# Kernel optimization log

Hardware: AMD Instinct MI355X
Metric: run time of the kernel (lower is better)

## Reference

```python
import jax, jax.numpy as jnp
import numpy as np

B, IN, OUT, E, H, K = 8192, 1024, 256, 16, 512, 3
EPS = 1e-10


def setup_inputs() -> dict:
    key = jax.random.key(0)
    ks = jax.random.split(key, 5)
    scaled = lambda k, shape, fan: jax.random.normal(k, shape, jnp.float32) / np.sqrt(fan)
    return {
        "x": jax.random.normal(ks[0], (B, IN), jnp.float32),
        # torch init is zeros for w_gate (degenerate ties); use small random for a meaningful reference
        "w_gate": jax.random.normal(ks[1], (IN, E), jnp.float32) * 0.02,
        "W1": scaled(ks[2], (E, IN, H), IN),
        "b1": jnp.zeros((E, H), jnp.float32),
        "W2": scaled(ks[3], (E, H, OUT), H),
        "b2": jnp.zeros((E, OUT), jnp.float32),
    }


def _cv_squared(v):
    # torch .var() is unbiased (ddof=1)
    return jnp.var(v, ddof=1) / (jnp.mean(v) ** 2 + EPS)


def reference(x, w_gate, W1, b1, W2, b2):
    # --- top-k gating (eval mode: clean logits, no noise) ---
    logits = x @ w_gate                                   # [B, E]
    top_vals, top_idx = jax.lax.top_k(logits, K)          # [B, K]
    top_gates = jax.nn.softmax(top_vals, axis=-1)         # softmax over selected k
    rows = jnp.arange(logits.shape[0])[:, None]
    gates = jnp.zeros_like(logits).at[rows, top_idx].set(top_gates)  # sparse gates [B, E]

    # --- load-balancing loss ---
    importance = gates.sum(0)
    load = (gates > 0).sum(0).astype(jnp.float32)         # _gates_to_load (eval path)
    loss = _cv_squared(importance) + _cv_squared(load)

    # --- experts (MLP stand-in; dense compute, sparse combine via zero gates) ---
    h = jax.nn.relu(jnp.einsum('bi,eih->beh', x, W1) + b1)  # [B, E, H]
    expert_out = jnp.einsum('beh,eho->beo', h, W2) + b2     # [B, E, OUT]

    # combine: equivalent to SparseDispatcher gather/split/scatter-add with gate weighting
    y = jnp.einsum('be,beo->bo', gates, expert_out)         # [B, OUT]
    return y, loss
```

## Files before the change

### kernel.cpp

```cpp
#include <hip/hip_runtime.h>

#define B_ 8192
#define IN_ 1024
#define OUT_ 256
#define E_ 16
#define KTOP 3
#define H_ 512
#define MAXSLOTS 26624
#define NTILES 208
#define HBLK 16

typedef __bf16 bf16;
typedef __bf16 bf16x4 __attribute__((ext_vector_type(4)));
typedef __bf16 bf16x8 __attribute__((ext_vector_type(8)));
typedef float f32x4 __attribute__((ext_vector_type(4)));

__device__ __forceinline__ void async16(const bf16* g, bf16* l) {
    __builtin_amdgcn_global_load_lds(
        (const __attribute__((address_space(1))) void*)g,
        (__attribute__((address_space(3))) void*)l,
        16, 0, 0);
}

__global__ __launch_bounds__(256) void k_init(
    int* __restrict__ row_ids, int* __restrict__ tile_expert,
    bf16* __restrict__ zero_row,
    const float* __restrict__ wg, float* __restrict__ wgT) {
    int id = blockIdx.x * 256 + threadIdx.x;
    if (id < MAXSLOTS) row_ids[id] = -1;
    if (id < NTILES) tile_expert[id] = -1;
    if (id < IN_) zero_row[id] = (bf16)0.f;
    if (id < E_ * IN_) {
        int e = id >> 10, j = id & 1023;
        wgT[id] = wg[j * E_ + e];
    }
}

__global__ __launch_bounds__(256) void k_transpose(
    const float* __restrict__ W1, bf16* __restrict__ w1t,
    const float* __restrict__ W2, bf16* __restrict__ w2t) {
    __shared__ float tile[64][65];
    int bx = blockIdx.x;
    const float* in; bf16* out; int Kd, Nd, e, tk, tn;
    if (bx < 2048) {
        in = W1; out = w1t; Kd = IN_; Nd = H_;
        e = bx >> 7; int tt = bx & 127; tk = tt >> 3; tn = tt & 7;
    } else {
        bx -= 2048;
        in = W2; out = w2t; Kd = H_; Nd = OUT_;
        e = bx >> 5; int tt = bx & 31; tk = tt >> 2; tn = tt & 3;
    }
    int t = threadIdx.x;
    int r = t >> 6, c = t & 63;
    const float* src = in + ((size_t)e * Kd + tk * 64) * Nd + (size_t)tn * 64;
#pragma unroll
    for (int i = 0; i < 16; i++) {
        int rr = r + i * 4;
        tile[rr][c] = src[(size_t)rr * Nd + c];
    }
    __syncthreads();
    bf16* dst = out + ((size_t)e * Nd + tn * 64) * Kd + (size_t)tk * 64;
#pragma unroll
    for (int i = 0; i < 16; i++) {
        int rr = r + i * 4;
        dst[(size_t)rr * Kd + c] = (bf16)tile[c][rr];
    }
}

__global__ __launch_bounds__(256) void k_gating(
    const float* __restrict__ x, const float* __restrict__ wgT,
    bf16* __restrict__ xbf, int* __restrict__ top_idx, float* __restrict__ top_gate) {
    int t = threadIdx.x;
    int row = blockIdx.x * 4 + (t >> 6);
    int lane = t & 63;
    float acc[16];
#pragma unroll
    for (int e = 0; e < 16; e++) acc[e] = 0.f;
    const float4* x4p = (const float4*)(x + (size_t)row * IN_);
    const float4* w4 = (const float4*)wgT;
#pragma unroll
    for (int it = 0; it < 4; it++) {
        int j0 = it * 64 + lane;
        float4 xv = x4p[j0];
        bf16x4 xb;
        xb[0] = (bf16)xv.x; xb[1] = (bf16)xv.y; xb[2] = (bf16)xv.z; xb[3] = (bf16)xv.w;
        *(bf16x4*)(xbf + (size_t)row * IN_ + j0 * 4) = xb;
#pragma unroll
        for (int e = 0; e < 16; e++) {
            float4 wv = w4[e * 256 + j0];
            acc[e] += xv.x * wv.x + xv.y * wv.y + xv.z * wv.z + xv.w * wv.w;
        }
    }
#pragma unroll
    for (int e = 0; e < 16; e++) {
#pragma unroll
        for (int s = 32; s > 0; s >>= 1) acc[e] += __shfl_xor(acc[e], s, 64);
    }
    if (lane == 0) {
        float v[16];
#pragma unroll
        for (int e = 0; e < 16; e++) v[e] = acc[e];
        int idx[KTOP];
        float val[KTOP];
#pragma unroll
        for (int k = 0; k < KTOP; k++) {
            int best = 0;
            float bv = v[0];
            for (int e = 1; e < 16; e++) {
                if (v[e] > bv) { bv = v[e]; best = e; }
            }
            idx[k] = best; val[k] = bv; v[best] = -1e30f;
        }
        float e1 = __expf(val[1] - val[0]);
        float e2 = __expf(val[2] - val[0]);
        float inv = 1.f / (1.f + e1 + e2);
        float g[KTOP] = {inv, e1 * inv, e2 * inv};
#pragma unroll
        for (int k = 0; k < KTOP; k++) {
            top_idx[row * KTOP + k] = idx[k];
            top_gate[row * KTOP + k] = g[k];
        }
    }
}

__global__ __launch_bounds__(256) void k_hist(
    const int* __restrict__ top_idx, int* __restrict__ partial) {
    __shared__ int wcnt[4][16];
    int t = threadIdx.x;
    int w = t >> 6, lane = t & 63;
    int blk = blockIdx.x;
    int cnt[16];
#pragma unroll
    for (int k = 0; k < 16; k++) cnt[k] = 0;
#pragma unroll
    for (int j = 0; j < 6; j++) {
        int e = top_idx[blk * 1536 + j * 256 + t];
#pragma unroll
        for (int k = 0; k < 16; k++)
            cnt[k] += (int)__popcll(__ballot(e == k));
    }
    if (lane == 0) {
#pragma unroll
        for (int k = 0; k < 16; k++) wcnt[w][k] = cnt[k];
    }
    __syncthreads();
    if (t < 16) partial[blk * 16 + t] = wcnt[0][t] + wcnt[1][t] + wcnt[2][t] + wcnt[3][t];
}

__global__ __launch_bounds__(256) void k_scan(
    const int* __restrict__ partial, int* __restrict__ counts,
    int* __restrict__ tile_expert, int* __restrict__ gbase) {
    __shared__ int sp[HBLK * 16];
    __shared__ int soff[16];
    int t = threadIdx.x;
    sp[t] = partial[t];
    __syncthreads();
    if (t < 16) {
        int s = 0;
#pragma unroll
        for (int b = 0; b < HBLK; b++) s += sp[b * 16 + t];
        counts[t] = s;
    }
    __syncthreads();
    if (t == 0) {
        int off = 0;
        for (int e = 0; e < E_; e++) {
            int c = 0;
#pragma unroll
            for (int b = 0; b < HBLK; b++) c += sp[b * 16 + e];
            soff[e] = off;
            int pd = (c + 127) & ~127;
            int t0 = off >> 7, t1 = (off + pd) >> 7;
            for (int tt = t0; tt < t1; ++tt) tile_expert[tt] = e;
            off += pd;
        }
    }
    __syncthreads();
    {
        int b = t >> 4, e = t & 15;
        int s = soff[e];
        for (int bp = 0; bp < b; bp++) s += sp[bp * 16 + e];
        gbase[t] = s;
    }
}

__global__ __launch_bounds__(256) void k_scatter(
    const int* __restrict__ top_idx, const float* __restrict__ top_gate,
    const int* __restrict__ gbase,
    int* __restrict__ row_ids, int* __restrict__ rowslot,
    float* __restrict__ partial_imp) {
    __shared__ int lcnt[16];
    __shared__ float limp[16];
    int t = threadIdx.x;
    int blk = blockIdx.x;
    if (t < 16) { lcnt[t] = 0; limp[t] = 0.f; }
    __syncthreads();
#pragma unroll
    for (int j = 0; j < 6; j++) {
        int gid = blk * 1536 + j * 256 + t;
        int e = top_idx[gid];
        float g = top_gate[gid];
        int rank = atomicAdd(&lcnt[e], 1);
        atomicAdd(&limp[e], g);
        int slot = gbase[blk * 16 + e] + rank;
        row_ids[slot] = gid / KTOP;
        rowslot[gid] = slot;
    }
    __syncthreads();
    if (t < 16) partial_imp[blk * 16 + t] = limp[t];
}


__global__ __launch_bounds__(256) void k_gemm1(
    const bf16* __restrict__ xbf, const bf16* __restrict__ w1t,
    const float* __restrict__ b1, const int* __restrict__ row_ids,
    const int* __restrict__ tile_expert, const bf16* __restrict__ zero_row,
    bf16* __restrict__ h) {
    int e = tile_expert[blockIdx.y];
    if (e < 0) return;
    int slot_base = blockIdx.y * 128;
    int nbase = blockIdx.x * 128;
    __shared__ __align__(16) bf16 As[128 * 64];
    __shared__ __align__(16) bf16 Bs[128 * 64];
    int t = threadIdx.x;
    int rmod = (t >> 3) & 7;
    int cglob = (t & 7) ^ rmod;
    const bf16* gA[4];
    const bf16* gB[4];
#pragma unroll
    for (int j = 0; j < 4; j++) {
        int m = j * 32 + (t >> 3);
        int rid = row_ids[slot_base + m];
        gA[j] = ((rid >= 0) ? xbf + (size_t)rid * IN_ : zero_row) + cglob * 8;
        gB[j] = w1t + ((size_t)e * H_ + nbase + m) * IN_ + cglob * 8;
    }
    int w = t >> 6, lane = t & 63;
    int wm = (w >> 1) * 64, wn = (w & 1) * 64;
    int lm = lane & 15, lq = lane >> 4;
    f32x4 acc[4][4] = {};
    for (int k0 = 0; k0 < IN_; k0 += 64) {
#pragma unroll
        for (int j = 0; j < 4; j++) {
            async16(gA[j] + k0, As + (j * 256 + t) * 8);
            async16(gB[j] + k0, Bs + (j * 256 + t) * 8);
        }
        __syncthreads();
        const bf16x8* Av = (const bf16x8*)As;
        const bf16x8* Bv = (const bf16x8*)Bs;
#pragma unroll
        for (int ks = 0; ks < 2; ks++) {
            int kc = ks * 4 + lq;
            bf16x8 af[4], bfv[4];
#pragma unroll
            for (int i = 0; i < 4; i++) {
                int row = wm + i * 16 + lm;
                af[i] = Av[row * 8 + (kc ^ (row & 7))];
            }
#pragma unroll
            for (int i = 0; i < 4; i++) {
                int row = wn + i * 16 + lm;
                bfv[i] = Bv[row * 8 + (kc ^ (row & 7))];
            }
#pragma unroll
            for (int mi = 0; mi < 4; mi++)
#pragma unroll
                for (int ni = 0; ni < 4; ni++)
                    acc[mi][ni] = __builtin_amdgcn_mfma_f32_16x16x32_bf16(af[mi], bfv[ni], acc[mi][ni], 0, 0, 0);
        }
        __syncthreads();
    }
#pragma unroll
    for (int mi = 0; mi < 4; mi++) {
#pragma unroll
        for (int ni = 0; ni < 4; ni++) {
            int colg = nbase + wn + ni * 16 + lm;
            float bias = b1[e * H_ + colg];
#pragma unroll
            for (int r = 0; r < 4; r++) {
                int rowl = wm + mi * 16 + lq * 4 + r;
                float v = acc[mi][ni][r] + bias;
                v = v > 0.f ? v : 0.f;
                h[(size_t)(slot_base + rowl) * H_ + colg] = (bf16)v;
            }
        }
    }
}

__global__ __launch_bounds__(256) void k_gemm2(
    const bf16* __restrict__ h, const bf16* __restrict__ w2t,
    const float* __restrict__ b2, const int* __restrict__ tile_expert,
    float* __restrict__ eout) {
    int e = tile_expert[blockIdx.y];
    if (e < 0) return;
    int slot_base = blockIdx.y * 128;
    int nbase = blockIdx.x * 128;
    __shared__ __align__(16) bf16 As[128 * 64];
    __shared__ __align__(16) bf16 Bs[128 * 64];
    int t = threadIdx.x;
    int rmod = (t >> 3) & 7;
    int cglob = (t & 7) ^ rmod;
    const bf16* gA[4];
    const bf16* gB[4];
#pragma unroll
    for (int j = 0; j < 4; j++) {
        int m = j * 32 + (t >> 3);
        gA[j] = h + (size_t)(slot_base + m) * H_ + cglob * 8;
        gB[j] = w2t + ((size_t)e * OUT_ + nbase + m) * H_ + cglob * 8;
    }
    int w = t >> 6, lane = t & 63;
    int wm = (w >> 1) * 64, wn = (w & 1) * 64;
    int lm = lane & 15, lq = lane >> 4;
    f32x4 acc[4][4] = {};
    for (int k0 = 0; k0 < H_; k0 += 64) {
#pragma unroll
        for (int j = 0; j < 4; j++) {
            async16(gA[j] + k0, As + (j * 256 + t) * 8);
            async16(gB[j] + k0, Bs + (j * 256 + t) * 8);
        }
        __syncthreads();
        const bf16x8* Av = (const bf16x8*)As;
        const bf16x8* Bv = (const bf16x8*)Bs;
#pragma unroll
        for (int ks = 0; ks < 2; ks++) {
            int kc = ks * 4 + lq;
            bf16x8 af[4], bfv[4];
#pragma unroll
            for (int i = 0; i < 4; i++) {
                int row = wm + i * 16 + lm;
                af[i] = Av[row * 8 + (kc ^ (row & 7))];
            }
#pragma unroll
            for (int i = 0; i < 4; i++) {
                int row = wn + i * 16 + lm;
                bfv[i] = Bv[row * 8 + (kc ^ (row & 7))];
            }
#pragma unroll
            for (int mi = 0; mi < 4; mi++)
#pragma unroll
                for (int ni = 0; ni < 4; ni++)
                    acc[mi][ni] = __builtin_amdgcn_mfma_f32_16x16x32_bf16(af[mi], bfv[ni], acc[mi][ni], 0, 0, 0);
        }
        __syncthreads();
    }
#pragma unroll
    for (int mi = 0; mi < 4; mi++) {
#pragma unroll
        for (int ni = 0; ni < 4; ni++) {
            int colg = nbase + wn + ni * 16 + lm;
            float bias = b2[e * OUT_ + colg];
#pragma unroll
            for (int r = 0; r < 4; r++) {
                int rowl = wm + mi * 16 + lq * 4 + r;
                eout[(size_t)(slot_base + rowl) * OUT_ + colg] = acc[mi][ni][r] + bias;
            }
        }
    }
}

__global__ __launch_bounds__(256) void k_combine(
    const float* __restrict__ eout, const int* __restrict__ rowslot,
    const float* __restrict__ top_gate, float* __restrict__ y) {
    int t = threadIdx.x;
    int b = blockIdx.x * 4 + (t >> 6);
    int lane = t & 63;
    int s0 = rowslot[b * 3], s1 = rowslot[b * 3 + 1], s2 = rowslot[b * 3 + 2];
    float g0 = top_gate[b * 3], g1 = top_gate[b * 3 + 1], g2 = top_gate[b * 3 + 2];
    const float4* e4 = (const float4*)eout;
    float4 v0 = e4[(size_t)s0 * 64 + lane];
    float4 v1 = e4[(size_t)s1 * 64 + lane];
    float4 v2 = e4[(size_t)s2 * 64 + lane];
    float4 r;
    r.x = g0 * v0.x + g1 * v1.x + g2 * v2.x;
    r.y = g0 * v0.y + g1 * v1.y + g2 * v2.y;
    r.z = g0 * v0.z + g1 * v1.z + g2 * v2.z;
    r.w = g0 * v0.w + g1 * v1.w + g2 * v2.w;
    ((float4*)y)[(size_t)b * 64 + lane] = r;
}

__global__ void k_loss(const float* __restrict__ partial_imp, const int* __restrict__ counts,
                       float* __restrict__ loss_out) {
    __shared__ float imp[16];
    int t = threadIdx.x;
    if (t < 16) {
        float s = 0.f;
#pragma unroll
        for (int b = 0; b < HBLK; b++) s += partial_imp[b * 16 + t];
        imp[t] = s;
    }
    __syncthreads();
    if (t == 0) {
        float si = 0.f, sl = 0.f;
        for (int e = 0; e < E_; e++) { si += imp[e]; sl += (float)counts[e]; }
        float mi_ = si / (float)E_, ml_ = sl / (float)E_;
        float vi = 0.f, vl = 0.f;
        for (int e = 0; e < E_; e++) {
            float d = imp[e] - mi_; vi += d * d;
            float d2 = (float)counts[e] - ml_; vl += d2 * d2;
        }
        vi /= (float)(E_ - 1); vl /= (float)(E_ - 1);
        *loss_out = vi / (mi_ * mi_ + 1e-10f) + vl / (ml_ * ml_ + 1e-10f);
    }
}

extern "C" void kernel_launch(void* const* d_in, const int* in_sizes, int n_in,
                              void* d_out, int out_size, void* d_ws, size_t ws_size,
                              hipStream_t stream) {
    (void)in_sizes; (void)n_in; (void)out_size; (void)ws_size;
    const float* x = (const float*)d_in[0];
    const float* wgate = (const float*)d_in[1];
    const float* W1 = (const float*)d_in[2];
    const float* b1 = (const float*)d_in[3];
    const float* W2 = (const float*)d_in[4];
    const float* b2 = (const float*)d_in[5];
    float* y = (float*)d_out;

    char* p = (char*)d_ws;
    auto alloc = [&](size_t bytes) {
        char* q = p;
        p += (bytes + 255) & ~(size_t)255;
        return q;
    };
    bf16* xbf = (bf16*)alloc((size_t)B_ * IN_ * 2);
    bf16* w1t = (bf16*)alloc((size_t)E_ * H_ * IN_ * 2);
    bf16* w2t = (bf16*)alloc((size_t)E_ * OUT_ * H_ * 2);
    bf16* h = (bf16*)alloc((size_t)MAXSLOTS * H_ * 2);
    int* row_ids = (int*)alloc((size_t)MAXSLOTS * 4);
    int* rowslot = (int*)alloc((size_t)B_ * KTOP * 4);
    int* top_idx = (int*)alloc((size_t)B_ * KTOP * 4);
    float* top_gate = (float*)alloc((size_t)B_ * KTOP * 4);
    int* counts = (int*)alloc(E_ * 4);
    int* partial = (int*)alloc(HBLK * E_ * 4);
    int* gbase = (int*)alloc(HBLK * E_ * 4);
    float* partial_imp = (float*)alloc(HBLK * E_ * 4);
    int* tile_expert = (int*)alloc(NTILES * 4);
    bf16* zero_row = (bf16*)alloc(IN_ * 2);
    float* wgT = (float*)alloc((size_t)E_ * IN_ * 4);
    float* eout = (float*)xbf;

    k_init<<<dim3((MAXSLOTS + 255) / 256), dim3(256), 0, stream>>>(
        row_ids, tile_expert, zero_row, wgate, wgT);
    k_transpose<<<dim3(2048 + 512), dim3(256), 0, stream>>>(W1, w1t, W2, w2t);
    k_gating<<<dim3(B_ / 4), dim3(256), 0, stream>>>(x, wgT, xbf, top_idx, top_gate);
    k_hist<<<dim3(HBLK), dim3(256), 0, stream>>>(top_idx, partial);
    k_scan<<<dim3(1), dim3(256), 0, stream>>>(partial, counts, tile_expert, gbase);
    k_scatter<<<dim3(HBLK), dim3(256), 0, stream>>>(
        top_idx, top_gate, gbase, row_ids, rowslot, partial_imp);
    k_gemm1<<<dim3(H_ / 128, NTILES), dim3(256), 0, stream>>>(
        xbf, w1t, b1, row_ids, tile_expert, zero_row, h);
    k_gemm2<<<dim3(OUT_ / 128, NTILES), dim3(256), 0, stream>>>(
        h, w2t, b2, tile_expert, eout);
    k_combine<<<dim3(B_ / 4), dim3(256), 0, stream>>>(eout, rowslot, top_gate, y);
    k_loss<<<dim3(1), dim3(64), 0, stream>>>(partial_imp, counts, y + (size_t)B_ * OUT_);
}
```

Baseline: 221.3 us.

## Merge setup kernels, widen gemm2 tile, store expert outputs as bf16, fold loss

```diff
diff --git a/kernel.cpp b/kernel.cpp
--- a/kernel.cpp
+++ b/kernel.cpp
@@ -22,35 +22,37 @@
         16, 0, 0);
 }
 
-__global__ __launch_bounds__(256) void k_init(
-    int* __restrict__ row_ids, int* __restrict__ tile_expert,
-    bf16* __restrict__ zero_row,
-    const float* __restrict__ wg, float* __restrict__ wgT) {
-    int id = blockIdx.x * 256 + threadIdx.x;
-    if (id < MAXSLOTS) row_ids[id] = -1;
-    if (id < NTILES) tile_expert[id] = -1;
-    if (id < IN_) zero_row[id] = (bf16)0.f;
-    if (id < E_ * IN_) {
-        int e = id >> 10, j = id & 1023;
-        wgT[id] = wg[j * E_ + e];
-    }
-}
-
-__global__ __launch_bounds__(256) void k_transpose(
+__global__ __launch_bounds__(256) void k_setup(
     const float* __restrict__ W1, bf16* __restrict__ w1t,
-    const float* __restrict__ W2, bf16* __restrict__ w2t) {
+    const float* __restrict__ W2, bf16* __restrict__ w2t,
+    int* __restrict__ row_ids, const float* __restrict__ wg, float* __restrict__ wgT,
+    bf16* __restrict__ zero_row, int* __restrict__ tile_expert) {
+    int bx = blockIdx.x;
+    int t = threadIdx.x;
+    if (bx >= 2560) {
+        if (bx < 2664) {
+            row_ids[(bx - 2560) * 256 + t] = -1;
+        } else if (bx < 2728) {
+            int id = (bx - 2664) * 256 + t;
+            int e = id >> 10, j = id & 1023;
+            wgT[id] = wg[j * E_ + e];
+        } else {
+#pragma unroll
+            for (int i = 0; i < 4; i++) zero_row[t * 4 + i] = (bf16)0.f;
+            if (t < NTILES) tile_expert[t] = -1;
+        }
+        return;
+    }
     __shared__ float tile[64][65];
-    int bx = blockIdx.x;
     const float* in; bf16* out; int Kd, Nd, e, tk, tn;
     if (bx < 2048) {
         in = W1; out = w1t; Kd = IN_; Nd = H_;
         e = bx >> 7; int tt = bx & 127; tk = tt >> 3; tn = tt & 7;
     } else {
-        bx -= 2048;
+        int b2x = bx - 2048;
         in = W2; out = w2t; Kd = H_; Nd = OUT_;
-        e = bx >> 5; int tt = bx & 31; tk = tt >> 2; tn = tt & 3;
-    }
-    int t = threadIdx.x;
+        e = b2x >> 5; int tt = b2x & 31; tk = tt >> 2; tn = tt & 3;
+    }
     int r = t >> 6, c = t & 63;
     const float* src = in + ((size_t)e * Kd + tk * 64) * Nd + (size_t)tn * 64;
 #pragma unroll
@@ -209,7 +211,6 @@
     __syncthreads();
     if (t < 16) partial_imp[blk * 16 + t] = limp[t];
 }
-
 
 __global__ __launch_bounds__(256) void k_gemm1(
     const bf16* __restrict__ xbf, const bf16* __restrict__ w1t,
@@ -289,55 +290,57 @@
 __global__ __launch_bounds__(256) void k_gemm2(
     const bf16* __restrict__ h, const bf16* __restrict__ w2t,
     const float* __restrict__ b2, const int* __restrict__ tile_expert,
-    float* __restrict__ eout) {
-    int e = tile_expert[blockIdx.y];
+    bf16* __restrict__ eout) {
+    int e = tile_expert[blockIdx.x];
     if (e < 0) return;
-    int slot_base = blockIdx.y * 128;
-    int nbase = blockIdx.x * 128;
+    int slot_base = blockIdx.x * 128;
     __shared__ __align__(16) bf16 As[128 * 64];
-    __shared__ __align__(16) bf16 Bs[128 * 64];
+    __shared__ __align__(16) bf16 Bs[256 * 64];
     int t = threadIdx.x;
     int rmod = (t >> 3) & 7;
     int cglob = (t & 7) ^ rmod;
     const bf16* gA[4];
-    const bf16* gB[4];
+    const bf16* gB[8];
 #pragma unroll
     for (int j = 0; j < 4; j++) {
         int m = j * 32 + (t >> 3);
         gA[j] = h + (size_t)(slot_base + m) * H_ + cglob * 8;
-        gB[j] = w2t + ((size_t)e * OUT_ + nbase + m) * H_ + cglob * 8;
+    }
+#pragma unroll
+    for (int j = 0; j < 8; j++) {
+        int m = j * 32 + (t >> 3);
+        gB[j] = w2t + ((size_t)e * OUT_ + m) * H_ + cglob * 8;
     }
     int w = t >> 6, lane = t & 63;
-    int wm = (w >> 1) * 64, wn = (w & 1) * 64;
+    int wm = (w >> 1) * 64, wn = (w & 1) * 128;
     int lm = lane & 15, lq = lane >> 4;
-    f32x4 acc[4][4] = {};
+    f32x4 acc[4][8] = {};
     for (int k0 = 0; k0 < H_; k0 += 64) {
 #pragma unroll
-        for (int j = 0; j < 4; j++) {
-            async16(gA[j] + k0, As + (j * 256 + t) * 8);
-            async16(gB[j] + k0, Bs + (j * 256 + t) * 8);
-        }
+        for (int j = 0; j < 4; j++) async16(gA[j] + k0, As + (j * 256 + t) * 8);
+#pragma unroll
+        for (int j = 0; j < 8; j++) async16(gB[j] + k0, Bs + (j * 256 + t) * 8);
         __syncthreads();
         const bf16x8* Av = (const bf16x8*)As;
         const bf16x8* Bv = (const bf16x8*)Bs;
 #pragma unroll
         for (int ks = 0; ks < 2; ks++) {
             int kc = ks * 4 + lq;
-            bf16x8 af[4], bfv[4];
+            bf16x8 af[4], bfv[8];
 #pragma unroll
             for (int i = 0; i < 4; i++) {
                 int row = wm + i * 16 + lm;
                 af[i] = Av[row * 8 + (kc ^ (row & 7))];
             }
 #pragma unroll
-            for (int i = 0; i < 4; i++) {
+            for (int i = 0; i < 8; i++) {
                 int row = wn + i * 16 + lm;
                 bfv[i] = Bv[row * 8 + (kc ^ (row & 7))];
             }
 #pragma unroll
             for (int mi = 0; mi < 4; mi++)
 #pragma unroll
-                for (int ni = 0; ni < 4; ni++)
+                for (int ni = 0; ni < 8; ni++)
                     acc[mi][ni] = __builtin_amdgcn_mfma_f32_16x16x32_bf16(af[mi], bfv[ni], acc[mi][ni], 0, 0, 0);
         }
         __syncthreads();
@@ -345,61 +348,60 @@
 #pragma unroll
     for (int mi = 0; mi < 4; mi++) {
 #pragma unroll
-        for (int ni = 0; ni < 4; ni++) {
-            int colg = nbase + wn + ni * 16 + lm;
+        for (int ni = 0; ni < 8; ni++) {
+            int colg = wn + ni * 16 + lm;
             float bias = b2[e * OUT_ + colg];
 #pragma unroll
             for (int r = 0; r < 4; r++) {
                 int rowl = wm + mi * 16 + lq * 4 + r;
-                eout[(size_t)(slot_base + rowl) * OUT_ + colg] = acc[mi][ni][r] + bias;
+                eout[(size_t)(slot_base + rowl) * OUT_ + colg] = (bf16)(acc[mi][ni][r] + bias);
             }
         }
     }
 }
 
 __global__ __launch_bounds__(256) void k_combine(
-    const float* __restrict__ eout, const int* __restrict__ rowslot,
-    const float* __restrict__ top_gate, float* __restrict__ y) {
-    int t = threadIdx.x;
+    const bf16* __restrict__ eout, const int* __restrict__ rowslot,
+    const float* __restrict__ top_gate, float* __restrict__ y,
+    const float* __restrict__ partial_imp, const int* __restrict__ counts,
+    float* __restrict__ loss_out) {
+    int t = threadIdx.x;
+    if (blockIdx.x == B_ / 4) {
+        __shared__ float imp[16];
+        if (t < 16) {
+            float s = 0.f;
+#pragma unroll
+            for (int b = 0; b < HBLK; b++) s += partial_imp[b * 16 + t];
+            imp[t] = s;
+        }
+        __syncthreads();
+        if (t == 0) {
+            float si = 0.f, sl = 0.f;
+            for (int e = 0; e < E_; e++) { si += imp[e]; sl += (float)counts[e]; }
+            float mi_ = si / (float)E_, ml_ = sl / (float)E_;
+            float vi = 0.f, vl = 0.f;
+            for (int e = 0; e < E_; e++) {
+                float d = imp[e] - mi_; vi += d * d;
+                float d2 = (float)counts[e] - ml_; vl += d2 * d2;
+            }
+            vi /= (float)(E_ - 1); vl /= (float)(E_ - 1);
+            *loss_out = vi / (mi_ * mi_ + 1e-10f) + vl / (ml_ * ml_ + 1e-10f);
+        }
+        return;
+    }
     int b = blockIdx.x * 4 + (t >> 6);
     int lane = t & 63;
     int s0 = rowslot[b * 3], s1 = rowslot[b * 3 + 1], s2 = rowslot[b * 3 + 2];
     float g0 = top_gate[b * 3], g1 = top_gate[b * 3 + 1], g2 = top_gate[b * 3 + 2];
-    const float4* e4 = (const float4*)eout;
-    float4 v0 = e4[(size_t)s0 * 64 + lane];
-    float4 v1 = e4[(size_t)s1 * 64 + lane];
-    float4 v2 = e4[(size_t)s2 * 64 + lane];
+    bf16x4 v0 = *(const bf16x4*)(eout + (size_t)s0 * OUT_ + lane * 4);
+    bf16x4 v1 = *(const bf16x4*)(eout + (size_t)s1 * OUT_ + lane * 4);
+    bf16x4 v2 = *(const bf16x4*)(eout + (size_t)s2 * OUT_ + lane * 4);
     float4 r;
-    r.x = g0 * v0.x + g1 * v1.x + g2 * v2.x;
-    r.y = g0 * v0.y + g1 * v1.y + g2 * v2.y;
-    r.z = g0 * v0.z + g1 * v1.z + g2 * v2.z;
-    r.w = g0 * v0.w + g1 * v1.w + g2 * v2.w;
+    r.x = g0 * (float)v0[0] + g1 * (float)v1[0] + g2 * (float)v2[0];
+    r.y = g0 * (float)v0[1] + g1 * (float)v1[1] + g2 * (float)v2[1];
+    r.z = g0 * (float)v0[2] + g1 * (float)v1[2] + g2 * (float)v2[2];
+    r.w = g0 * (float)v0[3] + g1 * (float)v1[3] + g2 * (float)v2[3];
     ((float4*)y)[(size_t)b * 64 + lane] = r;
-}
-
-__global__ void k_loss(const float* __restrict__ partial_imp, const int* __restrict__ counts,
-                       float* __restrict__ loss_out) {
-    __shared__ float imp[16];
-    int t = threadIdx.x;
-    if (t < 16) {
-        float s = 0.f;
-#pragma unroll
-        for (int b = 0; b < HBLK; b++) s += partial_imp[b * 16 + t];
-        imp[t] = s;
-    }
-    __syncthreads();
-    if (t == 0) {
-        float si = 0.f, sl = 0.f;
-        for (int e = 0; e < E_; e++) { si += imp[e]; sl += (float)counts[e]; }
-        float mi_ = si / (float)E_, ml_ = sl / (float)E_;
-        float vi = 0.f, vl = 0.f;
-        for (int e = 0; e < E_; e++) {
-            float d = imp[e] - mi_; vi += d * d;
-            float d2 = (float)counts[e] - ml_; vl += d2 * d2;
-        }
-        vi /= (float)(E_ - 1); vl /= (float)(E_ - 1);
-        *loss_out = vi / (mi_ * mi_ + 1e-10f) + vl / (ml_ * ml_ + 1e-10f);
-    }
 }
 
 extern "C" void kernel_launch(void* const* d_in, const int* in_sizes, int n_in,
@@ -435,11 +437,10 @@
     int* tile_expert = (int*)alloc(NTILES * 4);
     bf16* zero_row = (bf16*)alloc(IN_ * 2);
     float* wgT = (float*)alloc((size_t)E_ * IN_ * 4);
-    float* eout = (float*)xbf;
-
-    k_init<<<dim3((MAXSLOTS + 255) / 256), dim3(256), 0, stream>>>(
-        row_ids, tile_expert, zero_row, wgate, wgT);
-    k_transpose<<<dim3(2048 + 512), dim3(256), 0, stream>>>(W1, w1t, W2, w2t);
+    bf16* eout = (bf16*)xbf;
+
+    k_setup<<<dim3(2729), dim3(256), 0, stream>>>(
+        W1, w1t, W2, w2t, row_ids, wgate, wgT, zero_row, tile_expert);
     k_gating<<<dim3(B_ / 4), dim3(256), 0, stream>>>(x, wgT, xbf, top_idx, top_gate);
     k_hist<<<dim3(HBLK), dim3(256), 0, stream>>>(top_idx, partial);
     k_scan<<<dim3(1), dim3(256), 0, stream>>>(partial, counts, tile_expert, gbase);
@@ -447,8 +448,8 @@
         top_idx, top_gate, gbase, row_ids, rowslot, partial_imp);
     k_gemm1<<<dim3(H_ / 128, NTILES), dim3(256), 0, stream>>>(
         xbf, w1t, b1, row_ids, tile_expert, zero_row, h);
-    k_gemm2<<<dim3(OUT_ / 128, NTILES), dim3(256), 0, stream>>>(
+    k_gemm2<<<dim3(NTILES), dim3(256), 0, stream>>>(
         h, w2t, b2, tile_expert, eout);
-    k_combine<<<dim3(B_ / 4), dim3(256), 0, stream>>>(eout, rowslot, top_gate, y);
-    k_loss<<<dim3(1), dim3(64), 0, stream>>>(partial_imp, counts, y + (size_t)B_ * OUT_);
-}
+    k_combine<<<dim3(B_ / 4 + 1), dim3(256), 0, stream>>>(
+        eout, rowslot, top_gate, y, partial_imp, counts, y + (size_t)B_ * OUT_);
+}
```

Measured after the change: 219.4 us. Within noise of the previous version (-0.8%).
